# Kernel optimization log

Measured on AMD Instinct MI355X. Metric: run time of the kernel, lower is better.

The kernel has to match this reference:

```python
import jax, jax.numpy as jnp
import numpy as np
from jax import lax

IMG = 1024
STRIDES = (4, 8, 16, 32, 64)
SIZE_BASES = (32, 64, 128, 256, 512)
SCALES = (8.0,)
RATIOS = (0.5, 1.0, 2.0)
PRE_NMS = 2000
POST_NMS = 1000
NMS_THRESH = 0.7
B = 4


def _level_anchors(stride, size_base):
    """Anchors [G*G*A, 4] in xyxy, centered on grid cells."""
    g = IMG // stride
    cs = (jnp.arange(g, dtype=jnp.float32) + 0.5) * stride
    cy, cx = jnp.meshgrid(cs, cs, indexing='ij')          # [g,g]
    ctr = jnp.stack([cx.ravel(), cy.ravel()], axis=-1)    # [g*g, 2]
    wh = []
    for r in RATIOS:
        for s in SCALES:
            wh.append((size_base * s * np.sqrt(1.0 / r), size_base * s * np.sqrt(r)))
    wh = jnp.asarray(wh, jnp.float32)                     # [A, 2]
    x1y1 = ctr[:, None, :] - 0.5 * wh[None, :, :]
    x2y2 = ctr[:, None, :] + 0.5 * wh[None, :, :]
    return jnp.concatenate([x1y1, x2y2], axis=-1).reshape(-1, 4)


def _decode(anchors, deltas):
    wa = anchors[:, 2] - anchors[:, 0]
    ha = anchors[:, 3] - anchors[:, 1]
    cxa = anchors[:, 0] + 0.5 * wa
    cya = anchors[:, 1] + 0.5 * ha
    dx, dy, dw, dh = deltas[:, 0], deltas[:, 1], deltas[:, 2], deltas[:, 3]
    cx = dx * wa + cxa
    cy = dy * ha + cya
    w = jnp.exp(dw) * wa
    h = jnp.exp(dh) * ha
    return jnp.stack([cx - 0.5 * w, cy - 0.5 * h, cx + 0.5 * w, cy + 0.5 * h], axis=-1)


def _clip(boxes, info):
    h, w = info[0], info[1]
    x = jnp.clip(boxes[:, 0::2], 0.0, w - 1.0)
    y = jnp.clip(boxes[:, 1::2], 0.0, h - 1.0)
    return jnp.stack([x[:, 0], y[:, 0], x[:, 1], y[:, 1]], axis=-1)


def _iou_matrix(boxes):
    area = jnp.maximum(boxes[:, 2] - boxes[:, 0], 0.0) * jnp.maximum(boxes[:, 3] - boxes[:, 1], 0.0)
    lt = jnp.maximum(boxes[:, None, :2], boxes[None, :, :2])
    rb = jnp.minimum(boxes[:, None, 2:], boxes[None, :, 2:])
    wh = jnp.maximum(rb - lt, 0.0)
    inter = wh[..., 0] * wh[..., 1]
    return inter / jnp.maximum(area[:, None] + area[None, :] - inter, 1e-9)


def _nms_keep(boxes, thresh):
    """Boxes sorted by score desc. Returns boolean keep mask."""
    iou = _iou_matrix(boxes)
    n = boxes.shape[0]
    idx = jnp.arange(n)
    def body(i, keep):
        sup = keep[i] & (iou[i] > thresh) & (idx > i)
        return keep & ~sup
    return lax.fori_loop(0, n, body, jnp.ones((n,), bool))


def reference(probs0, probs1, probs2, probs3, probs4,
              reg0, reg1, reg2, reg3, reg4, img_info):
    anchors = [_level_anchors(s, b) for s, b in zip(STRIDES, SIZE_BASES)]
    probs = (probs0, probs1, probs2, probs3, probs4)
    regs = (reg0, reg1, reg2, reg3, reg4)

    def per_image(pr, rg, info):
        boxes_all, scores_all = [], []
        for a, p, r in zip(anchors, pr, rg):
            scores = p[:, 0]
            proposals = _clip(_decode(a, r), info)
            k = min(PRE_NMS, scores.shape[0])
            s, order = lax.top_k(scores, k)        # pre-NMS top-k, sorted desc
            bx = proposals[order]
            keep = _nms_keep(bx, NMS_THRESH)
            s = jnp.where(keep, s, -1.0)           # suppressed -> sentinel
            kp = min(POST_NMS, k)
            s2, o2 = lax.top_k(s, kp)              # post-NMS top-k per level
            boxes_all.append(bx[o2])
            scores_all.append(s2)
        ab = jnp.concatenate(boxes_all, axis=0)
        asc = jnp.concatenate(scores_all, axis=0)
        fs, fo = lax.top_k(asc, POST_NMS)          # merge levels, final top-k
        fb = jnp.where((fs >= 0.0)[:, None], ab[fo], 0.0)  # zero-pad invalid
        return fb

    fb = jax.vmap(per_image)(probs, regs, img_info)        # [B, POST, 4]
    bidx = jnp.broadcast_to(jnp.arange(B, dtype=fb.dtype)[:, None, None], (B, POST_NMS, 1))
    return jnp.concatenate([bidx, fb], axis=-1)            # [B, POST, 5]


def setup_inputs():
    key = jax.random.key(0)
    ks = jax.random.split(key, 10)
    grids = [IMG // s for s in STRIDES]
    A = [g * g * len(RATIOS) * len(SCALES) for g in grids]
    inp = {}
    for l in range(5):
        inp[f'probs{l}'] = jax.random.uniform(ks[l], (B, A[l], 2), dtype=jnp.float32)
        inp[f'reg{l}'] = 0.1 * jax.random.normal(ks[5 + l], (B, A[l], 4), dtype=jnp.float32)
    inp['img_info'] = jnp.tile(jnp.array([IMG, IMG, 1.0], jnp.float32), (B, 1))
    return inp
```

## Files before the change

kernel.cpp:

```cpp
#include <hip/hip_runtime.h>
#include <stdint.h>
#include <math.h>

#pragma clang fp contract(off)

#define NB 4
#define TOTA 261888
#define PRE 2000
#define POST 1000
#define CATN 4768
#define NBL 20
#define CANDCAP 4096
#define NBLK 4092
#define BPB 1023
#define HBLK 65

__device__ __forceinline__ unsigned keyF(float f) {
  unsigned u = __float_as_uint(f);
  return (u & 0x80000000u) ? ~u : (u | 0x80000000u);
}

__device__ __forceinline__ int lvlA(int l)   { switch (l) { case 0: return 196608; case 1: return 49152; case 2: return 12288; case 3: return 3072; default: return 768; } }
__device__ __forceinline__ int lvlOff(int l) { switch (l) { case 0: return 0; case 1: return 196608; case 2: return 245760; case 3: return 258048; default: return 261120; } }
__device__ __forceinline__ int lvlK(int l)   { return l == 4 ? 768 : 2000; }
__device__ __forceinline__ int lvlKP(int l)  { return l == 4 ? 768 : 1000; }
__device__ __forceinline__ int lvlBlkStart(int l) { switch (l) { case 0: return 0; case 1: return 768; case 2: return 960; case 3: return 1008; default: return 1020; } }
__device__ __forceinline__ int lvlBlkCnt(int l)   { switch (l) { case 0: return 768; case 1: return 192; case 2: return 48; case 3: return 12; default: return 3; } }

struct InPtrs {
  const float *p0, *p1, *p2, *p3, *p4;
  const float *r0, *r1, *r2, *r3, *r4;
  const float *info;
};

__device__ __forceinline__ void gaToLvl(int ga, int& l, int& off) {
  if (ga < 196608)      { l = 0; off = 0; }
  else if (ga < 245760) { l = 1; off = 196608; }
  else if (ga < 258048) { l = 2; off = 245760; }
  else if (ga < 261120) { l = 3; off = 258048; }
  else                  { l = 4; off = 261120; }
}

__device__ __forceinline__ void fatMap(int s, int& l, int& seg) {
  if (s < 48)      { l = 0; seg = s; }
  else if (s < 60) { l = 1; seg = s - 48; }
  else if (s < 63) { l = 2; seg = s - 60; }
  else if (s == 63){ l = 3; seg = 0; }
  else             { l = 4; seg = 0; }
}

__global__ __launch_bounds__(256) void k_decode(InPtrs P, float4* __restrict__ props,
                                                float* __restrict__ scores) {
  int gid = blockIdx.x * 256 + threadIdx.x;
  if (gid >= NB * TOTA) return;
  int b = gid / TOTA, ga = gid % TOTA;
  int Al, off, lg; float st; double S; const float *prp, *rgp;
  if (ga < 196608)      { Al = 196608; off = 0;      lg = 8; st = 4.0f;  S = 256.0;  prp = P.p0; rgp = P.r0; }
  else if (ga < 245760) { Al = 49152;  off = 196608; lg = 7; st = 8.0f;  S = 512.0;  prp = P.p1; rgp = P.r1; }
  else if (ga < 258048) { Al = 12288;  off = 245760; lg = 6; st = 16.0f; S = 1024.0; prp = P.p2; rgp = P.r2; }
  else if (ga < 261120) { Al = 3072;   off = 258048; lg = 5; st = 32.0f; S = 2048.0; prp = P.p3; rgp = P.r3; }
  else                  { Al = 768;    off = 261120; lg = 4; st = 64.0f; S = 4096.0; prp = P.p4; rgp = P.r4; }
  int i = ga - off;
  int cell = i / 3, rr = i - cell * 3;
  int col = cell & ((1 << lg) - 1), row = cell >> lg;
  float cx0 = ((float)col + 0.5f) * st;
  float cy0 = ((float)row + 0.5f) * st;
  const double SQ2 = 1.4142135623730951;
  const double SQH = 0.7071067811865476;
  double swd = (rr == 0) ? SQ2 : (rr == 1 ? 1.0 : SQH);
  double shd = (rr == 0) ? SQH : (rr == 1 ? 1.0 : SQ2);
  float wf = (float)(S * swd), hf = (float)(S * shd);
  float ax1 = cx0 - 0.5f * wf, ay1 = cy0 - 0.5f * hf;
  float ax2 = cx0 + 0.5f * wf, ay2 = cy0 + 0.5f * hf;
  size_t base = (size_t)b * Al + i;
  float sc = prp[base * 2];
  float4 d4 = ((const float4*)rgp)[base];
  float dx = d4.x, dy = d4.y, dw = d4.z, dh = d4.w;
  float wa = ax2 - ax1, ha = ay2 - ay1;
  float cxa = ax1 + 0.5f * wa, cya = ay1 + 0.5f * ha;
  float cx = dx * wa + cxa, cy = dy * ha + cya;
  float w = (float)exp((double)dw) * wa;
  float h = (float)exp((double)dh) * ha;
  float x1 = cx - 0.5f * w, y1 = cy - 0.5f * h;
  float x2 = cx + 0.5f * w, y2 = cy + 0.5f * h;
  float Hc = P.info[b * 3 + 0] - 1.0f, Wc = P.info[b * 3 + 1] - 1.0f;
  float4 o;
  o.x = fminf(fmaxf(x1, 0.0f), Wc);
  o.y = fminf(fmaxf(y1, 0.0f), Hc);
  o.z = fminf(fmaxf(x2, 0.0f), Wc);
  o.w = fminf(fmaxf(y2, 0.0f), Hc);
  props[gid] = o;
  scores[gid] = sc;
}

__global__ __launch_bounds__(256) void k_hist8(const float* __restrict__ scores,
                                               unsigned* __restrict__ hist8) {
  __shared__ unsigned h[256];
  int blk = blockIdx.x;
  int b = blk / HBLK, s = blk % HBLK;
  int l, seg; fatMap(s, l, seg);
  int n = lvlA(l), off = lvlOff(l);
  int start = seg * 4096;
  int cnt_s = min(4096, n - start);
  int tid = threadIdx.x;
  h[tid] = 0;
  __syncthreads();
  const float* sc = scores + (size_t)b * TOTA + off + start;
  for (int q = tid; q < cnt_s; q += 256)
    atomicAdd(&h[keyF(sc[q]) >> 24], 1u);
  __syncthreads();
  unsigned v = h[tid];
  if (v) atomicAdd(&hist8[(b * 5 + l) * 256 + tid], v);
}

__global__ __launch_bounds__(256) void k_thr8(const unsigned* __restrict__ hist8,
                                              unsigned* __restrict__ c1r1) {
  __shared__ unsigned h[256];
  int bl = blockIdx.x, tid = threadIdx.x;
  h[tid] = hist8[bl * 256 + tid];
  __syncthreads();
  if (tid == 0) {
    unsigned K = (unsigned)lvlK(bl % 5), cum = 0; int c;
    for (c = 255; c > 0; --c) { if (cum + h[c] >= K) break; cum += h[c]; }
    c1r1[bl * 2] = (unsigned)c;
    c1r1[bl * 2 + 1] = K - cum;
  }
}

__global__ __launch_bounds__(256) void k_hist6(const float* __restrict__ scores,
                                               const unsigned* __restrict__ c1r1,
                                               unsigned* __restrict__ hist6) {
  __shared__ unsigned h[64];
  int blk = blockIdx.x;
  int b = blk / HBLK, s = blk % HBLK;
  int l, seg; fatMap(s, l, seg);
  int n = lvlA(l), off = lvlOff(l);
  int start = seg * 4096;
  int cnt_s = min(4096, n - start);
  int tid = threadIdx.x;
  int bl = b * 5 + l;
  unsigned c1 = c1r1[bl * 2];
  if (tid < 64) h[tid] = 0;
  __syncthreads();
  const float* sc = scores + (size_t)b * TOTA + off + start;
  for (int q = tid; q < cnt_s; q += 256) {
    unsigned key = keyF(sc[q]);
    if ((key >> 24) == c1) atomicAdd(&h[(key >> 18) & 63u], 1u);
  }
  __syncthreads();
  if (tid < 64) {
    unsigned v = h[tid];
    if (v) atomicAdd(&hist6[bl * 64 + tid], v);
  }
}

__global__ __launch_bounds__(64) void k_thr6(const unsigned* __restrict__ hist6,
                                             const unsigned* __restrict__ c1r1,
                                             unsigned* __restrict__ T14) {
  __shared__ unsigned h[64];
  int bl = blockIdx.x, tid = threadIdx.x;
  h[tid] = hist6[bl * 64 + tid];
  __syncthreads();
  if (tid == 0) {
    unsigned r1 = c1r1[bl * 2 + 1], cum = 0; int c;
    for (c = 63; c > 0; --c) { if (cum + h[c] >= r1) break; cum += h[c]; }
    T14[bl] = (c1r1[bl * 2] << 6) | (unsigned)c;
  }
}

__global__ __launch_bounds__(256) void k_cnt(const float* __restrict__ scores,
                                             const unsigned* __restrict__ T14,
                                             unsigned* __restrict__ blockCnt) {
  __shared__ unsigned ws[4];
  int gid = blockIdx.x * 256 + threadIdx.x;
  int tid = threadIdx.x;
  int b = gid / TOTA, ga = gid % TOTA;
  int l, off; gaToLvl(ga, l, off);
  int bl = b * 5 + l;
  bool pred = (keyF(scores[gid]) >> 18) >= T14[bl];
  unsigned long long m = __ballot(pred);
  if ((tid & 63) == 0) ws[tid >> 6] = (unsigned)__popcll(m);
  __syncthreads();
  if (tid == 0) blockCnt[blockIdx.x] = ws[0] + ws[1] + ws[2] + ws[3];
}

__global__ __launch_bounds__(1024) void k_scanblk(const unsigned* __restrict__ blockCnt,
                                                  unsigned* __restrict__ blockBase,
                                                  unsigned* __restrict__ cnt) {
  __shared__ unsigned a[4096];
  __shared__ unsigned ch[1024];
  int tid = threadIdx.x;
  int q0 = tid * 4;
  unsigned a0 = (q0 + 0 < NBLK) ? blockCnt[q0 + 0] : 0u;
  unsigned a1 = (q0 + 1 < NBLK) ? blockCnt[q0 + 1] : 0u;
  unsigned a2 = (q0 + 2 < NBLK) ? blockCnt[q0 + 2] : 0u;
  unsigned a3 = (q0 + 3 < NBLK) ? blockCnt[q0 + 3] : 0u;
  unsigned p0 = a0, p1 = p0 + a1, p2 = p1 + a2, p3 = p2 + a3;
  ch[tid] = p3;
  __syncthreads();
  for (int d = 1; d < 1024; d <<= 1) {
    unsigned t = (tid >= d) ? ch[tid - d] : 0u;
    __syncthreads();
    ch[tid] += t;
    __syncthreads();
  }
  unsigned cbase = (tid > 0) ? ch[tid - 1] : 0u;
  a[q0 + 0] = cbase + p0;
  a[q0 + 1] = cbase + p1;
  a[q0 + 2] = cbase + p2;
  a[q0 + 3] = cbase + p3;
  __syncthreads();
  for (int k = 0; k < 4; ++k) {
    int g = q0 + k;
    if (g < NBLK) {
      int b = g / BPB, r = g % BPB;
      int l = (r < 768) ? 0 : (r < 960) ? 1 : (r < 1008) ? 2 : (r < 1020) ? 3 : 4;
      int ss = b * BPB + lvlBlkStart(l);
      unsigned Eg = (g > 0) ? a[g - 1] : 0u;
      unsigned Es = (ss > 0) ? a[ss - 1] : 0u;
      blockBase[g] = Eg - Es;
    }
  }
  if (tid < NBL) {
    int b = tid / 5, l = tid % 5;
    int ss = b * BPB + lvlBlkStart(l);
    int ee = ss + lvlBlkCnt(l);
    unsigned Ee = a[ee - 1];
    unsigned Es = (ss > 0) ? a[ss - 1] : 0u;
    cnt[tid] = Ee - Es;
  }
}

__global__ __launch_bounds__(256) void k_fill(const float* __restrict__ scores,
                                              const unsigned* __restrict__ T14,
                                              const unsigned* __restrict__ blockBase,
                                              unsigned long long* __restrict__ cand) {
  __shared__ unsigned ws[4];
  int gid = blockIdx.x * 256 + threadIdx.x;
  int tid = threadIdx.x;
  int b = gid / TOTA, ga = gid % TOTA;
  int l, off; gaToLvl(ga, l, off);
  int bl = b * 5 + l;
  unsigned key = keyF(scores[gid]);
  bool pred = (key >> 18) >= T14[bl];
  unsigned long long m = __ballot(pred);
  int wv = tid >> 6, ln = tid & 63;
  if (ln == 0) ws[wv] = (unsigned)__popcll(m);
  __syncthreads();
  unsigned wo = 0;
  for (int q = 0; q < wv; ++q) wo += ws[q];
  unsigned pre = (unsigned)__popcll(m & ((1ull << ln) - 1ull));
  if (pred) {
    unsigned p = blockBase[blockIdx.x] + wo + pre;
    if (p < CANDCAP)
      cand[(size_t)bl * CANDCAP + p] =
          ((unsigned long long)key << 32) | (unsigned long long)(0xFFFFFFFFu - (unsigned)(ga - off));
  }
}

__global__ __launch_bounds__(1024) void k_sort(const unsigned long long* __restrict__ cand,
                                               const unsigned* __restrict__ cnt,
                                               const float4* __restrict__ props,
                                               const float* __restrict__ scores,
                                               float4* __restrict__ sBox,
                                               float* __restrict__ sArea,
                                               float* __restrict__ sScore) {
  __shared__ unsigned long long arr[CANDCAP];
  int bl = blockIdx.x, b = bl / 5, l = bl % 5;
  int K = lvlK(l), off = lvlOff(l);
  int tid = threadIdx.x;
  int num = (int)min(cnt[bl], (unsigned)CANDCAP);
  for (int q = tid; q < CANDCAP; q += 1024)
    arr[q] = (q < num) ? cand[(size_t)bl * CANDCAP + q] : 0ull;
  __syncthreads();
  for (int kk = 2; kk <= CANDCAP; kk <<= 1)
    for (int jj = kk >> 1; jj > 0; jj >>= 1) {
      for (int idx = tid; idx < CANDCAP; idx += 1024) {
        int p2 = idx ^ jj;
        if (p2 > idx) {
          unsigned long long x = arr[idx], y = arr[p2];
          bool up = (idx & kk) == 0;
          if (up ? (x < y) : (x > y)) { arr[idx] = y; arr[p2] = x; }
        }
      }
      __syncthreads();
    }
  for (int j = tid; j < K; j += 1024) {
    unsigned long long e = arr[j];
    unsigned idx = 0xFFFFFFFFu - (unsigned)(e & 0xFFFFFFFFull);
    float4 bx = props[(size_t)b * TOTA + off + idx];
    float area = fmaxf(bx.z - bx.x, 0.0f) * fmaxf(bx.w - bx.y, 0.0f);
    sBox[bl * PRE + j] = bx;
    sArea[bl * PRE + j] = area;
    sScore[bl * PRE + j] = scores[(size_t)b * TOTA + off + idx];
  }
}

__global__ __launch_bounds__(256) void k_mask(const float4* __restrict__ sBox,
                                              const float* __restrict__ sArea,
                                              unsigned long long* __restrict__ mask) {
  int bi = blockIdx.x;
  int bl = bi >> 8, rem = bi & 255, ic = rem >> 3, wc = rem & 7;
  int l = bl % 5, K = lvlK(l);
  if (ic * 64 >= K) return;
  int tid = threadIdx.x;
  int j0 = wc * 256;
  int iL = tid >> 2, wL = tid & 3;
  int i = ic * 64 + iL;
  if (j0 + 255 <= ic * 64) {
    if (i < K) mask[((size_t)bl * PRE + i) * 32 + (wc * 4 + wL)] = 0ull;
    return;
  }
  __shared__ float4 jb[256];
  __shared__ float ja[256];
  {
    int j = j0 + tid;
    if (j < K) { jb[tid] = sBox[bl * PRE + j]; ja[tid] = sArea[bl * PRE + j]; }
    else { jb[tid] = make_float4(0.0f, 0.0f, 0.0f, 0.0f); ja[tid] = 0.0f; }
  }
  __syncthreads();
  if (i >= K) return;
  float4 a4 = sBox[bl * PRE + i];
  float ai = sArea[bl * PRE + i];
  unsigned long long bits = 0;
  int tb = wL * 64;
  for (int t = 0; t < 64; ++t) {
    int j = j0 + tb + t;
    if (j < K && j > i) {
      float4 b4 = jb[tb + t];
      float ltx = fmaxf(a4.x, b4.x), lty = fmaxf(a4.y, b4.y);
      float rbx = fminf(a4.z, b4.z), rby = fminf(a4.w, b4.w);
      float wx = fmaxf(rbx - ltx, 0.0f), wy = fmaxf(rby - lty, 0.0f);
      float inter = wx * wy;
      float den = fmaxf(ai + ja[tb + t] - inter, 1e-9f);
      float iou = inter / den;
      if (iou > 0.7f) bits |= (1ull << t);
    }
  }
  mask[((size_t)bl * PRE + i) * 32 + (wc * 4 + wL)] = bits;
}

__global__ __launch_bounds__(1024) void k_nms(const unsigned long long* __restrict__ mask,
                                              const float4* __restrict__ sBox,
                                              const float* __restrict__ sScore,
                                              float* __restrict__ catScore,
                                              float4* __restrict__ catBox) {
  __shared__ unsigned long long diag[PRE];
  __shared__ unsigned long long remv[32];
  __shared__ int list[1000];
  __shared__ int sTotal;
  int bl = blockIdx.x, b = bl / 5, l = bl % 5;
  int K = lvlK(l), KP = lvlKP(l), co = l * 1000;
  int tid = threadIdx.x;
  const unsigned long long* mrow = mask + (size_t)bl * PRE * 32;
  int c = tid & 31, g = tid >> 5;
  int nw = (K + 63) >> 6;
  for (int r = tid; r < K; r += 1024) diag[r] = mrow[(size_t)r * 32 + (r >> 6)];
  if (tid < 32) remv[tid] = 0ull;
  __syncthreads();
  unsigned long long w0 = 0ull, w1 = 0ull, nw0 = 0ull, nw1 = 0ull;
  {
    bool act = (c > 0) && (c < nw);
    int row0 = g, row1 = g + 32;
    if (act && row0 < K) w0 = mrow[(size_t)row0 * 32 + c];
    if (act && row1 < K) w1 = mrow[(size_t)row1 * 32 + c];
  }
  for (int t = 0; t < nw; ++t) {
    nw0 = 0ull; nw1 = 0ull;
    if (t + 1 < nw) {
      bool actn = (c > t + 1) && (c < nw);
      int row0 = (t + 1) * 64 + g, row1 = row0 + 32;
      if (actn && row0 < K) nw0 = mrow[(size_t)row0 * 32 + c];
      if (actn && row1 < K) nw1 = mrow[(size_t)row1 * 32 + c];
    }
    if (tid < 64) {
      int dr = t * 64 + tid;
      unsigned long long d = (dr < K) ? diag[dr] : 0ull;
      unsigned long long local = remv[t];
      int lim = min(64, K - t * 64);
      unsigned long long validm = (lim >= 64) ? ~0ull : ((1ull << lim) - 1ull);
      unsigned long long todo = (~local) & validm;
      while (todo) {
        int i2 = __ffsll((long long)todo) - 1;
        unsigned lo2 = __builtin_amdgcn_readlane((unsigned)d, i2);
        unsigned hi2 = __builtin_amdgcn_readlane((unsigned)(d >> 32), i2);
        unsigned long long dd = ((unsigned long long)hi2 << 32) | (unsigned long long)lo2;
        local |= dd;
        todo &= ~dd;
        todo &= ~(1ull << i2);
      }
      if (tid == 0) remv[t] = local;
    }
    __syncthreads();
    {
      unsigned long long local = remv[t];
      bool act = (c > t) && (c < nw);
      if (act) {
        unsigned long long acc = 0ull;
        int row0 = t * 64 + g, row1 = row0 + 32;
        if (row0 < K && !((local >> g) & 1ull)) acc |= w0;
        if (row1 < K && !((local >> (g + 32)) & 1ull)) acc |= w1;
        if (acc) atomicOr(&remv[c], acc);
      }
    }
    __syncthreads();
    w0 = nw0; w1 = nw1;
  }
  if (tid < 64) {
    int lane = tid;
    bool lv = lane < 32;
    unsigned long long remw = lv ? remv[lane] : 0ull;
    unsigned long long valid = 0ull;
    if (lv) {
      int rem = K - lane * 64;
      valid = (rem >= 64) ? ~0ull : (rem <= 0 ? 0ull : ((1ull << rem) - 1ull));
    }
    unsigned long long keepw = (~remw) & valid;
    unsigned long long suppw = remw & valid;
    unsigned long long lmask = (1ull << lane) - 1ull;
    int base = 0;
    for (int w2 = 0; w2 < 32 && base < KP; ++w2) {
      unsigned long long word = __shfl(keepw, w2);
      int pre = __popcll(word & lmask);
      if (((word >> lane) & 1ull) && (base + pre) < KP) list[base + pre] = w2 * 64 + lane;
      base += __popcll(word);
    }
    int totalKept = base;
    if (totalKept < KP) {
      int b2 = totalKept;
      for (int w2 = 0; w2 < 32 && b2 < KP; ++w2) {
        unsigned long long word = __shfl(suppw, w2);
        int pre = __popcll(word & lmask);
        if (((word >> lane) & 1ull) && (b2 + pre) < KP) list[b2 + pre] = w2 * 64 + lane;
        b2 += __popcll(word);
      }
    }
    if (lane == 0) sTotal = totalKept;
  }
  __syncthreads();
  int totalKept = sTotal;
  for (int t = tid; t < KP; t += 1024) {
    int j = list[t];
    float s = (t < totalKept) ? sScore[bl * PRE + j] : -1.0f;
    catScore[b * CATN + co + t] = s;
    catBox[b * CATN + co + t] = sBox[bl * PRE + j];
  }
}

__global__ __launch_bounds__(256) void k_final(const float* __restrict__ catScore,
                                               const float4* __restrict__ catBox,
                                               float* __restrict__ out) {
  int gid = blockIdx.x * 256 + threadIdx.x;
  if (gid >= NB * CATN) return;
  int b = gid / CATN, p = gid % CATN;
  int c = p / 1000; if (c > 4) c = 4;
  const float* cs = catScore + (size_t)b * CATN;
  float s = cs[p];
  unsigned long long me = ((unsigned long long)keyF(s) << 32) |
                          (unsigned long long)(0xFFFFFFFFu - (unsigned)p);
  int rank = p - c * 1000;
  for (int c2 = 0; c2 < 5; ++c2) {
    if (c2 == c) continue;
    int base = c2 * 1000, len = (c2 == 4) ? 768 : 1000;
    int lo = 0, hi = len;
    while (lo < hi) {
      int mid = (lo + hi) >> 1;
      int q = base + mid;
      unsigned long long k2 = ((unsigned long long)keyF(cs[q]) << 32) |
                              (unsigned long long)(0xFFFFFFFFu - (unsigned)q);
      if (k2 > me) lo = mid + 1; else hi = mid;
    }
    rank += lo;
  }
  if (rank < POST) {
    float4 bx = make_float4(0.0f, 0.0f, 0.0f, 0.0f);
    if (s >= 0.0f) bx = catBox[(size_t)b * CATN + p];
    float* o = out + ((size_t)b * POST + rank) * 5;
    o[0] = (float)b; o[1] = bx.x; o[2] = bx.y; o[3] = bx.z; o[4] = bx.w;
  }
}

extern "C" void kernel_launch(void* const* d_in, const int* in_sizes, int n_in,
                              void* d_out, int out_size, void* d_ws, size_t ws_size,
                              hipStream_t stream) {
  const int prSz[5] = {1572864, 393216, 98304, 24576, 6144};
  const int rgSz[5] = {3145728, 786432, 196608, 49152, 12288};
  const float* pr[5] = {nullptr, nullptr, nullptr, nullptr, nullptr};
  const float* rg[5] = {nullptr, nullptr, nullptr, nullptr, nullptr};
  const float* info = nullptr;
  for (int i = 0; i < n_in; ++i) {
    int s = in_sizes[i];
    bool m = false;
    for (int l = 0; l < 5; ++l) {
      if (s == prSz[l]) { pr[l] = (const float*)d_in[i]; m = true; break; }
      if (s == rgSz[l]) { rg[l] = (const float*)d_in[i]; m = true; break; }
    }
    if (!m && s == 12) info = (const float*)d_in[i];
  }
  InPtrs P;
  P.p0 = pr[0]; P.p1 = pr[1]; P.p2 = pr[2]; P.p3 = pr[3]; P.p4 = pr[4];
  P.r0 = rg[0]; P.r1 = rg[1]; P.r2 = rg[2]; P.r3 = rg[3]; P.r4 = rg[4];
  P.info = info;

  char* w = (char*)d_ws;
  float4* props = (float4*)w;                         w += (size_t)NB * TOTA * 16;
  float4* sBox = (float4*)w;                          w += (size_t)NBL * PRE * 16;
  float4* catBox = (float4*)w;                        w += (size_t)NB * CATN * 16;
  unsigned long long* mask = (unsigned long long*)w;  w += (size_t)NBL * PRE * 32 * 8;
  unsigned long long* cand = (unsigned long long*)w;  w += (size_t)NBL * CANDCAP * 8;
  float* scores = (float*)w;                          w += (size_t)NB * TOTA * 4;
  float* sArea = (float*)w;                           w += (size_t)NBL * PRE * 4;
  float* sScore = (float*)w;                          w += (size_t)NBL * PRE * 4;
  float* catScore = (float*)w;                        w += (size_t)NB * CATN * 4;
  unsigned* hist8 = (unsigned*)w;                     w += (size_t)NBL * 256 * 4;
  unsigned* hist6 = (unsigned*)w;                     w += (size_t)NBL * 64 * 4;
  unsigned* c1r1 = (unsigned*)w;                      w += (size_t)NBL * 2 * 4;
  unsigned* T14 = (unsigned*)w;                       w += (size_t)NBL * 4;
  unsigned* blockCnt = (unsigned*)w;                  w += (size_t)NBLK * 4;
  unsigned* blockBase = (unsigned*)w;                 w += (size_t)NBLK * 4;
  unsigned* cnt = (unsigned*)w;                       w += (size_t)NBL * 4;
  (void)ws_size; (void)out_size;

  hipMemsetAsync(hist8, 0, (size_t)NBL * (256 + 64) * 4, stream);

  k_decode<<<(NB * TOTA + 255) / 256, 256, 0, stream>>>(P, props, scores);
  k_hist8<<<NB * HBLK, 256, 0, stream>>>(scores, hist8);
  k_thr8<<<NBL, 256, 0, stream>>>(hist8, c1r1);
  k_hist6<<<NB * HBLK, 256, 0, stream>>>(scores, c1r1, hist6);
  k_thr6<<<NBL, 64, 0, stream>>>(hist6, c1r1, T14);
  k_cnt<<<NBLK, 256, 0, stream>>>(scores, T14, blockCnt);
  k_scanblk<<<1, 1024, 0, stream>>>(blockCnt, blockBase, cnt);
  k_fill<<<NBLK, 256, 0, stream>>>(scores, T14, blockBase, cand);
  k_sort<<<NBL, 1024, 0, stream>>>(cand, cnt, props, scores, sBox, sArea, sScore);
  k_mask<<<NBL * 256, 256, 0, stream>>>(sBox, sArea, mask);
  k_nms<<<NBL, 1024, 0, stream>>>(mask, sBox, sScore, catScore, catBox);
  k_final<<<(NB * CATN + 255) / 256, 256, 0, stream>>>(catScore, catBox, (float*)d_out);
}
```

Measured before the change: 237.3 us.

## Split per-level bitonic sort into chunk sorts plus binary-search merge ranking

The single 20-block, 4096-element bitonic sort is replaced by 160 blocks that each sort a 512-element chunk in shared memory, followed by a rank kernel. In the rank kernel each candidate binary-searches the other seven chunks to find its global position and scatters its box, area and score if that rank is below K. This spreads the sort over many more workgroups to cut the serial synchronisation-heavy stage. It adds one extra launch and global-memory binary searches. Ranks are distinct because the keys embed a unique index, so correctness holds.

After: 206.9 us. 12.8% less time.

```diff
diff --git a/kernel.cpp b/kernel.cpp
--- a/kernel.cpp
+++ b/kernel.cpp
@@ -258,24 +258,21 @@
   }
 }
 
-__global__ __launch_bounds__(1024) void k_sort(const unsigned long long* __restrict__ cand,
-                                               const unsigned* __restrict__ cnt,
-                                               const float4* __restrict__ props,
-                                               const float* __restrict__ scores,
-                                               float4* __restrict__ sBox,
-                                               float* __restrict__ sArea,
-                                               float* __restrict__ sScore) {
-  __shared__ unsigned long long arr[CANDCAP];
-  int bl = blockIdx.x, b = bl / 5, l = bl % 5;
-  int K = lvlK(l), off = lvlOff(l);
-  int tid = threadIdx.x;
+__global__ __launch_bounds__(256) void k_sortc(unsigned long long* __restrict__ cand,
+                                               const unsigned* __restrict__ cnt) {
+  __shared__ unsigned long long arr[512];
+  int blk = blockIdx.x;
+  int bl = blk >> 3, ch = blk & 7;
+  int base = ch * 512;
   int num = (int)min(cnt[bl], (unsigned)CANDCAP);
-  for (int q = tid; q < CANDCAP; q += 1024)
-    arr[q] = (q < num) ? cand[(size_t)bl * CANDCAP + q] : 0ull;
-  __syncthreads();
-  for (int kk = 2; kk <= CANDCAP; kk <<= 1)
+  int tid = threadIdx.x;
+  unsigned long long* cp = cand + (size_t)bl * CANDCAP + base;
+  for (int q = tid; q < 512; q += 256)
+    arr[q] = (base + q < num) ? cp[q] : 0ull;
+  __syncthreads();
+  for (int kk = 2; kk <= 512; kk <<= 1)
     for (int jj = kk >> 1; jj > 0; jj >>= 1) {
-      for (int idx = tid; idx < CANDCAP; idx += 1024) {
+      for (int idx = tid; idx < 512; idx += 256) {
         int p2 = idx ^ jj;
         if (p2 > idx) {
           unsigned long long x = arr[idx], y = arr[p2];
@@ -285,14 +282,40 @@
       }
       __syncthreads();
     }
-  for (int j = tid; j < K; j += 1024) {
-    unsigned long long e = arr[j];
-    unsigned idx = 0xFFFFFFFFu - (unsigned)(e & 0xFFFFFFFFull);
+  for (int q = tid; q < 512; q += 256) cp[q] = arr[q];
+}
+
+__global__ __launch_bounds__(256) void k_rank(const unsigned long long* __restrict__ cand,
+                                              const float4* __restrict__ props,
+                                              const float* __restrict__ scores,
+                                              float4* __restrict__ sBox,
+                                              float* __restrict__ sArea,
+                                              float* __restrict__ sScore) {
+  int gid = blockIdx.x * 256 + threadIdx.x;
+  int bl = gid >> 12, p = gid & 4095;
+  int b = bl / 5, l = bl % 5;
+  int K = lvlK(l), off = lvlOff(l);
+  const unsigned long long* cp = cand + (size_t)bl * CANDCAP;
+  unsigned long long me = cp[p];
+  int ch = p >> 9;
+  int rank = p & 511;
+  for (int c2 = 0; c2 < 8; ++c2) {
+    if (c2 == ch) continue;
+    const unsigned long long* d = cp + c2 * 512;
+    int lo = 0, hi = 512;
+    while (lo < hi) {
+      int mid = (lo + hi) >> 1;
+      if (d[mid] > me) lo = mid + 1; else hi = mid;
+    }
+    rank += lo;
+  }
+  if (rank < K) {
+    unsigned idx = 0xFFFFFFFFu - (unsigned)(me & 0xFFFFFFFFull);
     float4 bx = props[(size_t)b * TOTA + off + idx];
     float area = fmaxf(bx.z - bx.x, 0.0f) * fmaxf(bx.w - bx.y, 0.0f);
-    sBox[bl * PRE + j] = bx;
-    sArea[bl * PRE + j] = area;
-    sScore[bl * PRE + j] = scores[(size_t)b * TOTA + off + idx];
+    sBox[bl * PRE + rank] = bx;
+    sArea[bl * PRE + rank] = area;
+    sScore[bl * PRE + rank] = scores[(size_t)b * TOTA + off + idx];
   }
 }
 
@@ -531,7 +554,8 @@
   k_cnt<<<NBLK, 256, 0, stream>>>(scores, T14, blockCnt);
   k_scanblk<<<1, 1024, 0, stream>>>(blockCnt, blockBase, cnt);
   k_fill<<<NBLK, 256, 0, stream>>>(scores, T14, blockBase, cand);
-  k_sort<<<NBL, 1024, 0, stream>>>(cand, cnt, props, scores, sBox, sArea, sScore);
+  k_sortc<<<NBL * 8, 256, 0, stream>>>(cand, cnt);
+  k_rank<<<NBL * CANDCAP / 256, 256, 0, stream>>>(cand, props, scores, sBox, sArea, sScore);
   k_mask<<<NBL * 256, 256, 0, stream>>>(sBox, sArea, mask);
   k_nms<<<NBL, 1024, 0, stream>>>(mask, sBox, sScore, catScore, catBox);
   k_final<<<(NB * CATN + 255) / 256, 256, 0, stream>>>(catScore, catBox, (float*)d_out);
```
